# Performance work log

Hardware: AMD Instinct MI355X
Metric: run time of the kernel (lower is better)

Reference implementation:

```python
import jax, jax.numpy as jnp
import numpy as np


def setup_inputs() -> dict:
    key = jax.random.key(0)
    kq, kk, kv = jax.random.split(key, 3)
    S, D = 8192, 128
    return {
        "Q": jax.random.normal(kq, (S, D), dtype=jnp.float32),
        "K": jax.random.normal(kk, (S, D), dtype=jnp.float32),
        "V": jax.random.normal(kv, (S, D), dtype=jnp.float32),
    }


def reference(Q, K, V):
    d_k = Q.shape[-1]
    scale = 1.0 / jnp.sqrt(jnp.asarray(d_k, Q.dtype))
    scores = (Q @ K.T) * scale          # [S, S]
    attn = jax.nn.softmax(scores, axis=-1)
    return attn @ V                     # [S, Dv]
```

## Files before the change

kernel.cpp:

```cpp
#include <hip/hip_runtime.h>
#include <hip/hip_bf16.h>
#include <hip/hip_fp16.h>
#include <math.h>

typedef __attribute__((ext_vector_type(8))) short short8;
typedef __attribute__((ext_vector_type(16))) float f32x16;
typedef __attribute__((ext_vector_type(4))) unsigned short ushort4v;
typedef __attribute__((ext_vector_type(4))) unsigned int uint4v;

#define S 8192
#define D 128
#define QBLK 128
#define KVB 32

__device__ __forceinline__ unsigned short f2bf(float f) {
    unsigned int x = __float_as_uint(f);
    unsigned int r = x + 0x7fffu + ((x >> 16) & 1u);
    return (unsigned short)(r >> 16);
}

__device__ __forceinline__ unsigned int cvtpk(float a, float b) {
    unsigned int r;
    asm("v_cvt_pk_bf16_f32 %0, %1, %2" : "=v"(r) : "v"(a), "v"(b));
    return r;
}

__device__ __forceinline__ float fexp2(float x) { return __builtin_amdgcn_exp2f(x); }

__device__ __forceinline__ void gl_lds16(const unsigned short* g, unsigned short* l) {
    __builtin_amdgcn_global_load_lds(
        (const __attribute__((address_space(1))) unsigned int*)g,
        (__attribute__((address_space(3))) unsigned int*)l, 16, 0, 0);
}

__device__ __forceinline__ void plswap(unsigned int& a, unsigned int& b, int hi) {
#if __has_builtin(__builtin_amdgcn_permlane32_swap)
    auto r = __builtin_amdgcn_permlane32_swap((int)a, (int)b, false, false);
    a = (unsigned int)r[0];
    b = (unsigned int)r[1];
#else
    unsigned int xa = (unsigned int)__shfl_xor((int)a, 32, 64);
    unsigned int xb = (unsigned int)__shfl_xor((int)b, 32, 64);
    unsigned int na = hi ? xb : a;
    unsigned int nb = hi ? b : xa;
    a = na; b = nb;
#endif
}

union W4 { unsigned int u[4]; short8 v; };

__global__ __launch_bounds__(256) void prep_kv(const float* __restrict__ K,
                                               const float* __restrict__ V,
                                               unsigned short* __restrict__ Kb,
                                               unsigned short* __restrict__ Vf) {
    __shared__ unsigned short T[64][72];
    const float scale = 0.12751743022854459f;
    int s0 = blockIdx.x * 64, d0 = blockIdx.y * 64;
    int tr = threadIdx.x >> 4, tc = (threadIdx.x & 15) * 4;
#pragma unroll
    for (int p = 0; p < 4; ++p) {
        int r = p * 16 + tr;
        float4 kf = *reinterpret_cast<const float4*>(K + (size_t)(s0 + r) * D + d0 + tc);
        ushort4v ko = { f2bf(kf.x * scale), f2bf(kf.y * scale),
                        f2bf(kf.z * scale), f2bf(kf.w * scale) };
        *reinterpret_cast<ushort4v*>(Kb + (size_t)(s0 + r) * D + d0 + tc) = ko;
        float4 v = *reinterpret_cast<const float4*>(V + (size_t)(s0 + r) * D + d0 + tc);
        ushort4v vo = { f2bf(v.x), f2bf(v.y), f2bf(v.z), f2bf(v.w) };
        *reinterpret_cast<ushort4v*>(&T[r][tc]) = vo;
    }
    __syncthreads();
#pragma unroll
    for (int p = 0; p < 4; ++p) {
        int dr = p * 16 + tr;
        int d  = d0 + dr;
        int s  = s0 + tc;
        int t  = s >> 5;
        int ks = (s >> 3) & 3;
        int dt = d >> 5;
        int lane2 = (d & 31) | ((ks & 1) << 5);
        int f = dt * 2 + (ks >> 1);
        size_t idx = (((size_t)t * 8 + f) * 64 + lane2) * 8 + (s & 7);
        ushort4v o = { T[tc + 0][dr], T[tc + 1][dr], T[tc + 2][dr], T[tc + 3][dr] };
        *reinterpret_cast<ushort4v*>(Vf + idx) = o;
    }
}

#define QKOP(acc, kc) (acc) = __builtin_amdgcn_mfma_f32_32x32x16_bf16(              \
    *reinterpret_cast<const short8*>(                                               \
        &Kl[(size_t)c31 * 128 + (((2 * (kc) + hi) ^ (c31 & 15)) * 8)]),             \
    qf[kc], (acc), 0, 0, 0)

#define PVOPR(oo, pp, dt, off) (oo) = __builtin_amdgcn_mfma_f32_32x32x16_bf16(      \
    (pp).v, vr[(dt) * 2 + (off) / 2], (oo), 0, 0, 0)

#define LOADV do {                                                                   \
    _Pragma("unroll")                                                                \
    for (int f_ = 0; f_ < 8; ++f_)                                                   \
        vr[f_] = *reinterpret_cast<const short8*>(vfp + f_ * 512);                   \
    vfp += 4096;                                                                     \
} while (0)

#define SMEXG(g)                                                                     \
    {                                                                                \
        float e0 = fexp2(s[4 * (g) + 0]);                                            \
        float e1 = fexp2(s[4 * (g) + 1]);                                            \
        float e2 = fexp2(s[4 * (g) + 2]);                                            \
        float e3 = fexp2(s[4 * (g) + 3]);                                            \
        l_r += (e0 + e1) + (e2 + e3);                                                \
        wd[2 * (g) + 0] = cvtpk(e0, e1);                                             \
        wd[2 * (g) + 1] = cvtpk(e2, e3);                                             \
    }

#define SMFIN(PD0, PD1)                                                              \
    {                                                                                \
        plswap(wd[0], wd[2], hi); plswap(wd[1], wd[3], hi);                          \
        plswap(wd[4], wd[6], hi); plswap(wd[5], wd[7], hi);                          \
        PD0.u[0] = wd[0]; PD0.u[1] = wd[1]; PD0.u[2] = wd[2]; PD0.u[3] = wd[3];      \
        PD1.u[0] = wd[4]; PD1.u[1] = wd[5]; PD1.u[2] = wd[6]; PD1.u[3] = wd[7];      \
    }

#define STAGE_K(RING) do {                                                           \
    gl_lds16(kg[0], &Klds[RING][(w * 2 + 0) * 512]); kg[0] += (size_t)KVB * D;       \
    gl_lds16(kg[1], &Klds[RING][(w * 2 + 1) * 512]); kg[1] += (size_t)KVB * D;       \
} while (0)

#define PHASE_BARRIER() do {                                                         \
    asm volatile("s_waitcnt vmcnt(0)" ::: "memory");                                 \
    __builtin_amdgcn_s_barrier();                                                    \
    __builtin_amdgcn_sched_barrier(0);                                               \
} while (0)

#define SUBTILE(KR, PP0, PP1, QQ0, QQ1)                                              \
    {                                                                                \
        const unsigned short* Kl = Klds[KR];                                         \
        f32x16 s;                                                                    \
        _Pragma("unroll")                                                            \
        for (int i = 0; i < 16; ++i) s[i] = 0.f;                                     \
        __builtin_amdgcn_s_setprio(1);                                               \
        QKOP(s, 0); QKOP(s, 1); QKOP(s, 2); QKOP(s, 3);                              \
        QKOP(s, 4); QKOP(s, 5); QKOP(s, 6); QKOP(s, 7);                              \
        __builtin_amdgcn_s_setprio(0);                                               \
        unsigned int wd[8];                                                          \
        PVOPR(o0, PP0, 0, 0); PVOPR(o0, PP1, 0, 2); SMEXG(0);                        \
        PVOPR(o1, PP0, 1, 0); PVOPR(o1, PP1, 1, 2); SMEXG(1);                        \
        PVOPR(o2, PP0, 2, 0); PVOPR(o2, PP1, 2, 2); SMEXG(2);                        \
        PVOPR(o3, PP0, 3, 0); PVOPR(o3, PP1, 3, 2); SMEXG(3);                        \
        LOADV;                                                                       \
        SMFIN(QQ0, QQ1);                                                             \
    }

#define SUBTILE_NOPV(KR, QQ0, QQ1)                                                   \
    {                                                                                \
        const unsigned short* Kl = Klds[KR];                                         \
        f32x16 s;                                                                    \
        _Pragma("unroll")                                                            \
        for (int i = 0; i < 16; ++i) s[i] = 0.f;                                     \
        __builtin_amdgcn_s_setprio(1);                                               \
        QKOP(s, 0); QKOP(s, 1); QKOP(s, 2); QKOP(s, 3);                              \
        QKOP(s, 4); QKOP(s, 5); QKOP(s, 6); QKOP(s, 7);                              \
        __builtin_amdgcn_s_setprio(0);                                               \
        LOADV;                                                                       \
        unsigned int wd[8];                                                          \
        SMEXG(0); SMEXG(1); SMEXG(2); SMEXG(3);                                      \
        SMFIN(QQ0, QQ1);                                                             \
    }

__global__ __launch_bounds__(256, 2) void attn_fwd(
    const float* __restrict__ Q, const unsigned short* __restrict__ Kb,
    const unsigned short* __restrict__ Vf, float* __restrict__ out,
    __half* __restrict__ wsO, float* __restrict__ wsL, int split)
{
    __shared__ __attribute__((aligned(16))) unsigned short Klds[4][KVB * D];

    const int tid  = threadIdx.x;
    const int w    = tid >> 6;
    const int lane = tid & 63;
    const int hi   = lane >> 5;
    const int c31  = lane & 31;
    const int bid  = blockIdx.x;
    const int sp   = bid % split;
    const int qb   = bid / split;
    const int chunk  = S / split;
    const int kv0    = sp * chunk;
    const int ntiles = chunk / KVB;

    short8 qf[8];
    {
        const float* qrow = Q + (size_t)(qb * QBLK + w * 32 + c31) * D;
#pragma unroll
        for (int kc = 0; kc < 8; ++kc) {
            float4 x = *reinterpret_cast<const float4*>(qrow + kc * 16 + hi * 8);
            float4 y = *reinterpret_cast<const float4*>(qrow + kc * 16 + hi * 8 + 4);
            W4 u;
            u.u[0] = cvtpk(x.x, x.y); u.u[1] = cvtpk(x.z, x.w);
            u.u[2] = cvtpk(y.x, y.y); u.u[3] = cvtpk(y.z, y.w);
            qf[kc] = u.v;
        }
    }

    const unsigned short* kg[2];
#pragma unroll
    for (int i = 0; i < 2; ++i) {
        int krow = w * 8 + i * 4 + (lane >> 4);
        int kch  = (lane & 15) ^ (krow & 15);
        kg[i] = Kb + (size_t)(kv0 + krow) * D + kch * 8;
    }

    const unsigned short* vfp = Vf + (size_t)(kv0 >> 5) * 4096 + (size_t)lane * 8;
    short8 vr[8];

    f32x16 o0, o1, o2, o3;
#pragma unroll
    for (int i = 0; i < 16; ++i) { o0[i] = 0.f; o1[i] = 0.f; o2[i] = 0.f; o3[i] = 0.f; }
    float l_r = 0.f;
    W4 pX0, pX1, pY0, pY1;

    STAGE_K(0); STAGE_K(1);

    PHASE_BARRIER();
    STAGE_K(2); STAGE_K(3);
    SUBTILE_NOPV(0, pY0, pY1);
    SUBTILE(1, pY0, pY1, pX0, pX1);

    const int npair = ntiles / 4 - 1;
#pragma unroll 1
    for (int j = 0; j < npair; ++j) {
        PHASE_BARRIER();
        STAGE_K(0); STAGE_K(1);
        SUBTILE(2, pX0, pX1, pY0, pY1);
        SUBTILE(3, pY0, pY1, pX0, pX1);
        PHASE_BARRIER();
        STAGE_K(2); STAGE_K(3);
        SUBTILE(0, pX0, pX1, pY0, pY1);
        SUBTILE(1, pY0, pY1, pX0, pX1);
    }

    PHASE_BARRIER();
    SUBTILE(2, pX0, pX1, pY0, pY1);
    SUBTILE(3, pY0, pY1, pX0, pX1);

    {
        __builtin_amdgcn_s_setprio(1);
        PVOPR(o0, pX0, 0, 0); PVOPR(o0, pX1, 0, 2);
        PVOPR(o1, pX0, 1, 0); PVOPR(o1, pX1, 1, 2);
        PVOPR(o2, pX0, 2, 0); PVOPR(o2, pX1, 2, 2);
        PVOPR(o3, pX0, 3, 0); PVOPR(o3, pX1, 3, 2);
        __builtin_amdgcn_s_setprio(0);
    }

    float l_tot = l_r + __shfl_xor(l_r, 32, 64);
    if (split == 1) {
#pragma unroll
        for (int reg = 0; reg < 16; ++reg) {
            int crow = (reg & 3) + 8 * (reg >> 2) + 4 * hi;
            float lr  = __shfl(l_tot, crow, 64);
            float inv = 1.f / lr;
            size_t rb = (size_t)(qb * QBLK + w * 32 + crow) * D;
            out[rb +  0 + c31] = o0[reg] * inv;
            out[rb + 32 + c31] = o1[reg] * inv;
            out[rb + 64 + c31] = o2[reg] * inv;
            out[rb + 96 + c31] = o3[reg] * inv;
        }
    } else {
        __half* Opart = wsO + (size_t)(qb * split + sp) * (QBLK * D);
#pragma unroll
        for (int reg = 0; reg < 16; ++reg) {
            int crow = (reg & 3) + 8 * (reg >> 2) + 4 * hi;
            size_t rb = (size_t)(w * 32 + crow) * D;
            Opart[rb +  0 + c31] = __float2half(o0[reg]);
            Opart[rb + 32 + c31] = __float2half(o1[reg]);
            Opart[rb + 64 + c31] = __float2half(o2[reg]);
            Opart[rb + 96 + c31] = __float2half(o3[reg]);
        }
        if (hi == 0)
            wsL[(size_t)(qb * split + sp) * QBLK + w * 32 + c31] = l_tot;
    }
}

__global__ void attn_combine(const __half* __restrict__ wsO,
                             const float* __restrict__ wsL,
                             float* __restrict__ out, int split)
{
    int idx = blockIdx.x * blockDim.x + threadIdx.x;
    if (idx >= S * D / 8) return;
    int row = idx >> 4;
    int g   = (idx & 15) * 8;
    int qb = row >> 7, rloc = row & 127;
    float acc[8];
#pragma unroll
    for (int i = 0; i < 8; ++i) acc[i] = 0.f;
    float L = 0.f;
    for (int s = 0; s < split; ++s) {
        size_t b = (size_t)(qb * split + s);
        const __half* p = wsO + b * (QBLK * D) + (size_t)rloc * D + g;
        uint4v u = *reinterpret_cast<const uint4v*>(p);
#pragma unroll
        for (int i = 0; i < 4; ++i) {
            unsigned int wbits = u[i];
            __half2 h = *reinterpret_cast<__half2*>(&wbits);
            float2 f = __half22float2(h);
            acc[2 * i]     += f.x;
            acc[2 * i + 1] += f.y;
        }
        L += wsL[b * QBLK + rloc];
    }
    float inv = 1.f / L;
    size_t ob = (size_t)row * D + g;
    float4 w0 = { acc[0] * inv, acc[1] * inv, acc[2] * inv, acc[3] * inv };
    float4 w1 = { acc[4] * inv, acc[5] * inv, acc[6] * inv, acc[7] * inv };
    *reinterpret_cast<float4*>(out + ob)     = w0;
    *reinterpret_cast<float4*>(out + ob + 4) = w1;
}

extern "C" void kernel_launch(void* const* d_in, const int* in_sizes, int n_in,
                              void* d_out, int out_size, void* d_ws, size_t ws_size,
                              hipStream_t stream) {
    const float* Q = (const float*)d_in[0];
    const float* K = (const float*)d_in[1];
    const float* V = (const float*)d_in[2];
    float* out = (float*)d_out;

    size_t base = 2ull * S * D * sizeof(unsigned short);
    int split = 1;
    for (int sp = 16; sp >= 2; sp >>= 1) {
        size_t need = base + (size_t)sp * S * D * sizeof(__half)
                    + (size_t)sp * S * sizeof(float);
        if (ws_size >= need) { split = sp; break; }
    }

    unsigned short* Kb = (unsigned short*)d_ws;
    unsigned short* Vf = Kb + (size_t)S * D;
    __half* wsO = (__half*)(Vf + (size_t)S * D);
    float* wsL = (float*)(wsO + (size_t)split * S * D);

    prep_kv<<<dim3(S / 64, D / 64), 256, 0, stream>>>(K, V, Kb, Vf);
    attn_fwd<<<(S / QBLK) * split, 256, 0, stream>>>(Q, Kb, Vf, out, wsO, wsL, split);
    if (split > 1)
        attn_combine<<<(S * D / 8 + 255) / 256, 256, 0, stream>>>(wsO, wsL, out, split);
}
```

Measured before the change: 61.43 us.

## Double-buffer V registers, delay K staging past first subtile, cap split at 8

Splits the V register fragment into even and odd buffers so the V load for the next tile is issued a full subtile earlier. The barrier now waits with vmcnt(8) instead of draining all memory ops. K staging moves to between the two subtiles, fenced by sched barriers. To afford the extra registers, occupancy drops from 2 blocks to 1 per CU, and the maximum KV split falls from 16 to 8. This trades occupancy and split parallelism for deeper software prefetch.

```diff
diff --git a/kernel.cpp b/kernel.cpp
--- a/kernel.cpp
+++ b/kernel.cpp
@@ -90,13 +90,13 @@
         &Kl[(size_t)c31 * 128 + (((2 * (kc) + hi) ^ (c31 & 15)) * 8)]),             \
     qf[kc], (acc), 0, 0, 0)
 
-#define PVOPR(oo, pp, dt, off) (oo) = __builtin_amdgcn_mfma_f32_32x32x16_bf16(      \
-    (pp).v, vr[(dt) * 2 + (off) / 2], (oo), 0, 0, 0)
-
-#define LOADV do {                                                                   \
+#define PVOPR(oo, pp, dt, off, VR) (oo) = __builtin_amdgcn_mfma_f32_32x32x16_bf16(  \
+    (pp).v, VR[(dt) * 2 + (off) / 2], (oo), 0, 0, 0)
+
+#define LOADV(VR) do {                                                               \
     _Pragma("unroll")                                                                \
     for (int f_ = 0; f_ < 8; ++f_)                                                   \
-        vr[f_] = *reinterpret_cast<const short8*>(vfp + f_ * 512);                   \
+        VR[f_] = *reinterpret_cast<const short8*>(vfp + f_ * 512);                   \
     vfp += 4096;                                                                     \
 } while (0)
 
@@ -124,13 +124,19 @@
     gl_lds16(kg[1], &Klds[RING][(w * 2 + 1) * 512]); kg[1] += (size_t)KVB * D;       \
 } while (0)
 
-#define PHASE_BARRIER() do {                                                         \
-    asm volatile("s_waitcnt vmcnt(0)" ::: "memory");                                 \
+#define STAGE_K2(RA, RB) do {                                                        \
+    __builtin_amdgcn_sched_barrier(0);                                               \
+    STAGE_K(RA); STAGE_K(RB);                                                        \
+    __builtin_amdgcn_sched_barrier(0);                                               \
+} while (0)
+
+#define PHASE_BARRIER8() do {                                                        \
+    asm volatile("s_waitcnt vmcnt(8)" ::: "memory");                                 \
     __builtin_amdgcn_s_barrier();                                                    \
     __builtin_amdgcn_sched_barrier(0);                                               \
 } while (0)
 
-#define SUBTILE(KR, PP0, PP1, QQ0, QQ1)                                              \
+#define SUBTILE(KR, PP0, PP1, QQ0, QQ1, VR)                                          \
     {                                                                                \
         const unsigned short* Kl = Klds[KR];                                         \
         f32x16 s;                                                                    \
@@ -141,15 +147,16 @@
         QKOP(s, 4); QKOP(s, 5); QKOP(s, 6); QKOP(s, 7);                              \
         __builtin_amdgcn_s_setprio(0);                                               \
         unsigned int wd[8];                                                          \
-        PVOPR(o0, PP0, 0, 0); PVOPR(o0, PP1, 0, 2); SMEXG(0);                        \
-        PVOPR(o1, PP0, 1, 0); PVOPR(o1, PP1, 1, 2); SMEXG(1);                        \
-        PVOPR(o2, PP0, 2, 0); PVOPR(o2, PP1, 2, 2); SMEXG(2);                        \
-        PVOPR(o3, PP0, 3, 0); PVOPR(o3, PP1, 3, 2); SMEXG(3);                        \
-        LOADV;                                                                       \
+        PVOPR(o0, PP0, 0, 0, VR); PVOPR(o0, PP1, 0, 2, VR); SMEXG(0);                \
+        PVOPR(o1, PP0, 1, 0, VR); PVOPR(o1, PP1, 1, 2, VR); SMEXG(1);                \
+        PVOPR(o2, PP0, 2, 0, VR); PVOPR(o2, PP1, 2, 2, VR); SMEXG(2);                \
+        PVOPR(o3, PP0, 3, 0, VR); PVOPR(o3, PP1, 3, 2, VR); SMEXG(3);                \
+        LOADV(VR);                                                                   \
+        __builtin_amdgcn_sched_barrier(0);                                           \
         SMFIN(QQ0, QQ1);                                                             \
     }
 
-#define SUBTILE_NOPV(KR, QQ0, QQ1)                                                   \
+#define SUBTILE_NL(KR, PP0, PP1, QQ0, QQ1, VR)                                       \
     {                                                                                \
         const unsigned short* Kl = Klds[KR];                                         \
         f32x16 s;                                                                    \
@@ -159,13 +166,32 @@
         QKOP(s, 0); QKOP(s, 1); QKOP(s, 2); QKOP(s, 3);                              \
         QKOP(s, 4); QKOP(s, 5); QKOP(s, 6); QKOP(s, 7);                              \
         __builtin_amdgcn_s_setprio(0);                                               \
-        LOADV;                                                                       \
+        unsigned int wd[8];                                                          \
+        PVOPR(o0, PP0, 0, 0, VR); PVOPR(o0, PP1, 0, 2, VR); SMEXG(0);                \
+        PVOPR(o1, PP0, 1, 0, VR); PVOPR(o1, PP1, 1, 2, VR); SMEXG(1);                \
+        PVOPR(o2, PP0, 2, 0, VR); PVOPR(o2, PP1, 2, 2, VR); SMEXG(2);                \
+        PVOPR(o3, PP0, 3, 0, VR); PVOPR(o3, PP1, 3, 2, VR); SMEXG(3);                \
+        SMFIN(QQ0, QQ1);                                                             \
+    }
+
+#define SUBTILE_NOPV(KR, QQ0, QQ1, VR)                                               \
+    {                                                                                \
+        const unsigned short* Kl = Klds[KR];                                         \
+        f32x16 s;                                                                    \
+        _Pragma("unroll")                                                            \
+        for (int i = 0; i < 16; ++i) s[i] = 0.f;                                     \
+        __builtin_amdgcn_s_setprio(1);                                               \
+        QKOP(s, 0); QKOP(s, 1); QKOP(s, 2); QKOP(s, 3);                              \
+        QKOP(s, 4); QKOP(s, 5); QKOP(s, 6); QKOP(s, 7);                              \
+        __builtin_amdgcn_s_setprio(0);                                               \
+        LOADV(VR);                                                                   \
+        __builtin_amdgcn_sched_barrier(0);                                           \
         unsigned int wd[8];                                                          \
         SMEXG(0); SMEXG(1); SMEXG(2); SMEXG(3);                                      \
         SMFIN(QQ0, QQ1);                                                             \
     }
 
-__global__ __launch_bounds__(256, 2) void attn_fwd(
+__global__ __launch_bounds__(256, 1) void attn_fwd(
     const float* __restrict__ Q, const unsigned short* __restrict__ Kb,
     const unsigned short* __restrict__ Vf, float* __restrict__ out,
     __half* __restrict__ wsO, float* __restrict__ wsL, int split)
@@ -207,7 +233,7 @@
     }
 
     const unsigned short* vfp = Vf + (size_t)(kv0 >> 5) * 4096 + (size_t)lane * 8;
-    short8 vr[8];
+    short8 vrE[8], vrO[8];
 
     f32x16 o0, o1, o2, o3;
 #pragma unroll
@@ -216,35 +242,38 @@
     W4 pX0, pX1, pY0, pY1;
 
     STAGE_K(0); STAGE_K(1);
-
-    PHASE_BARRIER();
-    STAGE_K(2); STAGE_K(3);
-    SUBTILE_NOPV(0, pY0, pY1);
-    SUBTILE(1, pY0, pY1, pX0, pX1);
+    __builtin_amdgcn_sched_barrier(0);
+    LOADV(vrE);
+    __builtin_amdgcn_sched_barrier(0);
+
+    PHASE_BARRIER8();
+    SUBTILE_NOPV(0, pY0, pY1, vrO);
+    STAGE_K2(2, 3);
+    SUBTILE(1, pY0, pY1, pX0, pX1, vrE);
 
     const int npair = ntiles / 4 - 1;
 #pragma unroll 1
     for (int j = 0; j < npair; ++j) {
-        PHASE_BARRIER();
-        STAGE_K(0); STAGE_K(1);
-        SUBTILE(2, pX0, pX1, pY0, pY1);
-        SUBTILE(3, pY0, pY1, pX0, pX1);
-        PHASE_BARRIER();
-        STAGE_K(2); STAGE_K(3);
-        SUBTILE(0, pX0, pX1, pY0, pY1);
-        SUBTILE(1, pY0, pY1, pX0, pX1);
-    }
-
-    PHASE_BARRIER();
-    SUBTILE(2, pX0, pX1, pY0, pY1);
-    SUBTILE(3, pY0, pY1, pX0, pX1);
+        PHASE_BARRIER8();
+        SUBTILE(2, pX0, pX1, pY0, pY1, vrO);
+        STAGE_K2(0, 1);
+        SUBTILE(3, pY0, pY1, pX0, pX1, vrE);
+        PHASE_BARRIER8();
+        SUBTILE(0, pX0, pX1, pY0, pY1, vrO);
+        STAGE_K2(2, 3);
+        SUBTILE(1, pY0, pY1, pX0, pX1, vrE);
+    }
+
+    PHASE_BARRIER8();
+    SUBTILE(2, pX0, pX1, pY0, pY1, vrO);
+    SUBTILE_NL(3, pY0, pY1, pX0, pX1, vrE);
 
     {
         __builtin_amdgcn_s_setprio(1);
-        PVOPR(o0, pX0, 0, 0); PVOPR(o0, pX1, 0, 2);
-        PVOPR(o1, pX0, 1, 0); PVOPR(o1, pX1, 1, 2);
-        PVOPR(o2, pX0, 2, 0); PVOPR(o2, pX1, 2, 2);
-        PVOPR(o3, pX0, 3, 0); PVOPR(o3, pX1, 3, 2);
+        PVOPR(o0, pX0, 0, 0, vrO); PVOPR(o0, pX1, 0, 2, vrO);
+        PVOPR(o1, pX0, 1, 0, vrO); PVOPR(o1, pX1, 1, 2, vrO);
+        PVOPR(o2, pX0, 2, 0, vrO); PVOPR(o2, pX1, 2, 2, vrO);
+        PVOPR(o3, pX0, 3, 0, vrO); PVOPR(o3, pX1, 3, 2, vrO);
         __builtin_amdgcn_s_setprio(0);
     }
 
@@ -322,7 +351,7 @@
 
     size_t base = 2ull * S * D * sizeof(unsigned short);
     int split = 1;
-    for (int sp = 16; sp >= 2; sp >>= 1) {
+    for (int sp = 8; sp >= 2; sp >>= 1) {
         size_t need = base + (size_t)sp * S * D * sizeof(__half)
                     + (size_t)sp * S * sizeof(float);
         if (ws_size >= need) { split = sp; break; }
```

After: 66.81 us. 1.09x slower.

## Load K fragments directly into registers instead of staging through LDS

Applied to the files above, without the earlier changes.

Removes the LDS ring buffer and global-to-LDS staging for K, along with the per-phase barriers. K is instead pre-permuted into MFMA fragment order in the prep kernel and loaded per wave straight into registers, the same way V already is. QK accumulation is split into two accumulators to shorten MFMA dependency chains, and occupancy hint and max split are lowered. Each wave now fetches K independently, which raises global/L2 traffic and register pressure, and no loads are shared across waves.

```diff
diff --git a/kernel.cpp b/kernel.cpp
--- a/kernel.cpp
+++ b/kernel.cpp
@@ -26,12 +26,6 @@
 }
 
 __device__ __forceinline__ float fexp2(float x) { return __builtin_amdgcn_exp2f(x); }
-
-__device__ __forceinline__ void gl_lds16(const unsigned short* g, unsigned short* l) {
-    __builtin_amdgcn_global_load_lds(
-        (const __attribute__((address_space(1))) unsigned int*)g,
-        (__attribute__((address_space(3))) unsigned int*)l, 16, 0, 0);
-}
 
 __device__ __forceinline__ void plswap(unsigned int& a, unsigned int& b, int hi) {
 #if __has_builtin(__builtin_amdgcn_permlane32_swap)
@@ -51,7 +45,7 @@
 
 __global__ __launch_bounds__(256) void prep_kv(const float* __restrict__ K,
                                                const float* __restrict__ V,
-                                               unsigned short* __restrict__ Kb,
+                                               unsigned short* __restrict__ Kf,
                                                unsigned short* __restrict__ Vf) {
     __shared__ unsigned short T[64][72];
     const float scale = 0.12751743022854459f;
@@ -60,11 +54,20 @@
 #pragma unroll
     for (int p = 0; p < 4; ++p) {
         int r = p * 16 + tr;
-        float4 kf = *reinterpret_cast<const float4*>(K + (size_t)(s0 + r) * D + d0 + tc);
+        int rg = s0 + r;
+        float4 kf = *reinterpret_cast<const float4*>(K + (size_t)rg * D + d0 + tc);
         ushort4v ko = { f2bf(kf.x * scale), f2bf(kf.y * scale),
                         f2bf(kf.z * scale), f2bf(kf.w * scale) };
-        *reinterpret_cast<ushort4v*>(Kb + (size_t)(s0 + r) * D + d0 + tc) = ko;
-        float4 v = *reinterpret_cast<const float4*>(V + (size_t)(s0 + r) * D + d0 + tc);
+        {
+            int c0 = d0 + tc;
+            int t  = rg >> 5;
+            int rr = rg & 31;
+            int kc = c0 >> 4;
+            int hp = (c0 >> 3) & 1;
+            size_t idx = (((size_t)t * 8 + kc) * 64 + rr + 32 * hp) * 8 + (c0 & 7);
+            *reinterpret_cast<ushort4v*>(Kf + idx) = ko;
+        }
+        float4 v = *reinterpret_cast<const float4*>(V + (size_t)rg * D + d0 + tc);
         ushort4v vo = { f2bf(v.x), f2bf(v.y), f2bf(v.z), f2bf(v.w) };
         *reinterpret_cast<ushort4v*>(&T[r][tc]) = vo;
     }
@@ -85,13 +88,18 @@
     }
 }
 
-#define QKOP(acc, kc) (acc) = __builtin_amdgcn_mfma_f32_32x32x16_bf16(              \
-    *reinterpret_cast<const short8*>(                                               \
-        &Kl[(size_t)c31 * 128 + (((2 * (kc) + hi) ^ (c31 & 15)) * 8)]),             \
-    qf[kc], (acc), 0, 0, 0)
+#define QKR(acc, kc) (acc) = __builtin_amdgcn_mfma_f32_32x32x16_bf16(               \
+    kr[kc], qf[kc], (acc), 0, 0, 0)
 
 #define PVOPR(oo, pp, dt, off) (oo) = __builtin_amdgcn_mfma_f32_32x32x16_bf16(      \
     (pp).v, vr[(dt) * 2 + (off) / 2], (oo), 0, 0, 0)
+
+#define LOADK do {                                                                   \
+    _Pragma("unroll")                                                                \
+    for (int f_ = 0; f_ < 8; ++f_)                                                   \
+        kr[f_] = *reinterpret_cast<const short8*>(kfp + f_ * 512);                   \
+    kfp += 4096;                                                                     \
+} while (0)
 
 #define LOADV do {                                                                   \
     _Pragma("unroll")                                                                \
@@ -102,10 +110,10 @@
 
 #define SMEXG(g)                                                                     \
     {                                                                                \
-        float e0 = fexp2(s[4 * (g) + 0]);                                            \
-        float e1 = fexp2(s[4 * (g) + 1]);                                            \
-        float e2 = fexp2(s[4 * (g) + 2]);                                            \
-        float e3 = fexp2(s[4 * (g) + 3]);                                            \
+        float e0 = fexp2(sa[4 * (g) + 0] + sb[4 * (g) + 0]);                         \
+        float e1 = fexp2(sa[4 * (g) + 1] + sb[4 * (g) + 1]);                         \
+        float e2 = fexp2(sa[4 * (g) + 2] + sb[4 * (g) + 2]);                         \
+        float e3 = fexp2(sa[4 * (g) + 3] + sb[4 * (g) + 3]);                         \
         l_r += (e0 + e1) + (e2 + e3);                                                \
         wd[2 * (g) + 0] = cvtpk(e0, e1);                                             \
         wd[2 * (g) + 1] = cvtpk(e2, e3);                                             \
@@ -119,26 +127,33 @@
         PD1.u[0] = wd[4]; PD1.u[1] = wd[5]; PD1.u[2] = wd[6]; PD1.u[3] = wd[7];      \
     }
 
-#define STAGE_K(RING) do {                                                           \
-    gl_lds16(kg[0], &Klds[RING][(w * 2 + 0) * 512]); kg[0] += (size_t)KVB * D;       \
-    gl_lds16(kg[1], &Klds[RING][(w * 2 + 1) * 512]); kg[1] += (size_t)KVB * D;       \
-} while (0)
-
-#define PHASE_BARRIER() do {                                                         \
-    asm volatile("s_waitcnt vmcnt(0)" ::: "memory");                                 \
-    __builtin_amdgcn_s_barrier();                                                    \
-    __builtin_amdgcn_sched_barrier(0);                                               \
-} while (0)
-
-#define SUBTILE(KR, PP0, PP1, QQ0, QQ1)                                              \
-    {                                                                                \
-        const unsigned short* Kl = Klds[KR];                                         \
-        f32x16 s;                                                                    \
+#define SUBTILE(PP0, PP1, QQ0, QQ1)                                                  \
+    {                                                                                \
+        f32x16 sa, sb;                                                               \
         _Pragma("unroll")                                                            \
-        for (int i = 0; i < 16; ++i) s[i] = 0.f;                                     \
+        for (int i = 0; i < 16; ++i) { sa[i] = 0.f; sb[i] = 0.f; }                   \
         __builtin_amdgcn_s_setprio(1);                                               \
-        QKOP(s, 0); QKOP(s, 1); QKOP(s, 2); QKOP(s, 3);                              \
-        QKOP(s, 4); QKOP(s, 5); QKOP(s, 6); QKOP(s, 7);                              \
+        QKR(sa, 0); QKR(sb, 1); QKR(sa, 2); QKR(sb, 3);                              \
+        QKR(sa, 4); QKR(sb, 5); QKR(sa, 6); QKR(sb, 7);                              \
+        __builtin_amdgcn_s_setprio(0);                                               \
+        LOADK;                                                                       \
+        unsigned int wd[8];                                                          \
+        PVOPR(o0, PP0, 0, 0); PVOPR(o0, PP1, 0, 2); SMEXG(0);                        \
+        PVOPR(o1, PP0, 1, 0); PVOPR(o1, PP1, 1, 2); SMEXG(1);                        \
+        PVOPR(o2, PP0, 2, 0); PVOPR(o2, PP1, 2, 2); SMEXG(2);                        \
+        PVOPR(o3, PP0, 3, 0); PVOPR(o3, PP1, 3, 2); SMEXG(3);                        \
+        LOADV;                                                                       \
+        SMFIN(QQ0, QQ1);                                                             \
+    }
+
+#define SUBTILE_NK(PP0, PP1, QQ0, QQ1)                                               \
+    {                                                                                \
+        f32x16 sa, sb;                                                               \
+        _Pragma("unroll")                                                            \
+        for (int i = 0; i < 16; ++i) { sa[i] = 0.f; sb[i] = 0.f; }                   \
+        __builtin_amdgcn_s_setprio(1);                                               \
+        QKR(sa, 0); QKR(sb, 1); QKR(sa, 2); QKR(sb, 3);                              \
+        QKR(sa, 4); QKR(sb, 5); QKR(sa, 6); QKR(sb, 7);                              \
         __builtin_amdgcn_s_setprio(0);                                               \
         unsigned int wd[8];                                                          \
         PVOPR(o0, PP0, 0, 0); PVOPR(o0, PP1, 0, 2); SMEXG(0);                        \
@@ -149,29 +164,27 @@
         SMFIN(QQ0, QQ1);                                                             \
     }
 
-#define SUBTILE_NOPV(KR, QQ0, QQ1)                                                   \
-    {                                                                                \
-        const unsigned short* Kl = Klds[KR];                                         \
-        f32x16 s;                                                                    \
+#define SUBTILE0(QQ0, QQ1)                                                           \
+    {                                                                                \
+        f32x16 sa, sb;                                                               \
         _Pragma("unroll")                                                            \
-        for (int i = 0; i < 16; ++i) s[i] = 0.f;                                     \
+        for (int i = 0; i < 16; ++i) { sa[i] = 0.f; sb[i] = 0.f; }                   \
         __builtin_amdgcn_s_setprio(1);                                               \
-        QKOP(s, 0); QKOP(s, 1); QKOP(s, 2); QKOP(s, 3);                              \
-        QKOP(s, 4); QKOP(s, 5); QKOP(s, 6); QKOP(s, 7);                              \
+        QKR(sa, 0); QKR(sb, 1); QKR(sa, 2); QKR(sb, 3);                              \
+        QKR(sa, 4); QKR(sb, 5); QKR(sa, 6); QKR(sb, 7);                              \
         __builtin_amdgcn_s_setprio(0);                                               \
+        LOADK;                                                                       \
         LOADV;                                                                       \
         unsigned int wd[8];                                                          \
         SMEXG(0); SMEXG(1); SMEXG(2); SMEXG(3);                                      \
         SMFIN(QQ0, QQ1);                                                             \
     }
 
-__global__ __launch_bounds__(256, 2) void attn_fwd(
-    const float* __restrict__ Q, const unsigned short* __restrict__ Kb,
+__global__ __launch_bounds__(256, 1) void attn_fwd(
+    const float* __restrict__ Q, const unsigned short* __restrict__ Kf,
     const unsigned short* __restrict__ Vf, float* __restrict__ out,
     __half* __restrict__ wsO, float* __restrict__ wsL, int split)
 {
-    __shared__ __attribute__((aligned(16))) unsigned short Klds[4][KVB * D];
-
     const int tid  = threadIdx.x;
     const int w    = tid >> 6;
     const int lane = tid & 63;
@@ -198,16 +211,9 @@
         }
     }
 
-    const unsigned short* kg[2];
-#pragma unroll
-    for (int i = 0; i < 2; ++i) {
-        int krow = w * 8 + i * 4 + (lane >> 4);
-        int kch  = (lane & 15) ^ (krow & 15);
-        kg[i] = Kb + (size_t)(kv0 + krow) * D + kch * 8;
-    }
-
+    const unsigned short* kfp = Kf + (size_t)(kv0 >> 5) * 4096 + (size_t)lane * 8;
     const unsigned short* vfp = Vf + (size_t)(kv0 >> 5) * 4096 + (size_t)lane * 8;
-    short8 vr[8];
+    short8 kr[8], vr[8];
 
     f32x16 o0, o1, o2, o3;
 #pragma unroll
@@ -215,29 +221,18 @@
     float l_r = 0.f;
     W4 pX0, pX1, pY0, pY1;
 
-    STAGE_K(0); STAGE_K(1);
-
-    PHASE_BARRIER();
-    STAGE_K(2); STAGE_K(3);
-    SUBTILE_NOPV(0, pY0, pY1);
-    SUBTILE(1, pY0, pY1, pX0, pX1);
-
-    const int npair = ntiles / 4 - 1;
+    LOADK;
+
+    SUBTILE0(pY0, pY1);
+
+    const int npair = (ntiles - 2) / 2;
 #pragma unroll 1
     for (int j = 0; j < npair; ++j) {
-        PHASE_BARRIER();
-        STAGE_K(0); STAGE_K(1);
-        SUBTILE(2, pX0, pX1, pY0, pY1);
-        SUBTILE(3, pY0, pY1, pX0, pX1);
-        PHASE_BARRIER();
-        STAGE_K(2); STAGE_K(3);
-        SUBTILE(0, pX0, pX1, pY0, pY1);
-        SUBTILE(1, pY0, pY1, pX0, pX1);
-    }
-
-    PHASE_BARRIER();
-    SUBTILE(2, pX0, pX1, pY0, pY1);
-    SUBTILE(3, pY0, pY1, pX0, pX1);
+        SUBTILE(pY0, pY1, pX0, pX1);
+        SUBTILE(pX0, pX1, pY0, pY1);
+    }
+
+    SUBTILE_NK(pY0, pY1, pX0, pX1);
 
     {
         __builtin_amdgcn_s_setprio(1);
@@ -322,19 +317,19 @@
 
     size_t base = 2ull * S * D * sizeof(unsigned short);
     int split = 1;
-    for (int sp = 16; sp >= 2; sp >>= 1) {
+    for (int sp = 8; sp >= 2; sp >>= 1) {
         size_t need = base + (size_t)sp * S * D * sizeof(__half)
                     + (size_t)sp * S * sizeof(float);
         if (ws_size >= need) { split = sp; break; }
     }
 
-    unsigned short* Kb = (unsigned short*)d_ws;
-    unsigned short* Vf = Kb + (size_t)S * D;
+    unsigned short* Kf = (unsigned short*)d_ws;
+    unsigned short* Vf = Kf + (size_t)S * D;
     __half* wsO = (__half*)(Vf + (size_t)S * D);
     float* wsL = (float*)(wsO + (size_t)split * S * D);
 
-    prep_kv<<<dim3(S / 64, D / 64), 256, 0, stream>>>(K, V, Kb, Vf);
-    attn_fwd<<<(S / QBLK) * split, 256, 0, stream>>>(Q, Kb, Vf, out, wsO, wsL, split);
+    prep_kv<<<dim3(S / 64, D / 64), 256, 0, stream>>>(K, V, Kf, Vf);
+    attn_fwd<<<(S / QBLK) * split, 256, 0, stream>>>(Q, Kf, Vf, out, wsO, wsL, split);
     if (split > 1)
         attn_combine<<<(S * D / 8 + 255) / 256, 256, 0, stream>>>(wsO, wsL, out, split);
 }
```

Result: slower. 64.00 us (+4.2%).
